# Kernel tuning notes

Measured on AMD Instinct MI355X. Metric: run time of the kernel, lower is better.

The kernel has to match this reference:

```python
import jax, jax.numpy as jnp
import numpy as np

BN_EPS = 1e-5


def _conv1x1(w, x):
    # w: [out, in], x: [B, in, N] -> [B, out, N]
    return jnp.einsum('oi,bin->bon', w, x)


def _bn_eval(x, g, b, m, v):
    # x: [B, C, N]; eval-mode BatchNorm1d with running stats
    scale = (g / jnp.sqrt(v + BN_EPS))[None, :, None]
    shift = (b - m * g / jnp.sqrt(v + BN_EPS))[None, :, None]
    return x * scale + shift


def _sa_layer(x, xyz, wqk, wv, bvv, wt, btt, g, b2, m, v):
    # offset-attention (SALayerCLS). q_conv and k_conv share weights -> q == k.
    h = x + xyz                                   # [B, C, N]
    q = _conv1x1(wqk, h)                          # [B, C//4, N]
    val = _conv1x1(wv, h) + bvv[None, :, None]    # [B, C, N]
    energy = jnp.einsum('bdn,bdm->bnm', q, q)     # [B, N, N]
    att = jax.nn.softmax(energy, axis=-1)
    # double normalization: L1-renormalize over dim=1 (rows)
    att = att / (1e-9 + att.sum(axis=1, keepdims=True))
    x_r = jnp.einsum('bcn,bnm->bcm', val, att)    # [B, C, N]
    t = _conv1x1(wt, x - x_r) + btt[None, :, None]
    t = jax.nn.relu(_bn_eval(t, g, b2, m, v))
    return x + t


def setup_inputs() -> dict:
    key = jax.random.key(0)
    ks = jax.random.split(key, 17)
    B, C, N = 8, 256, 2048
    f = jnp.float32
    return {
        'x': jax.random.normal(ks[0], (B, C, N), f),
        'xyz': jax.random.normal(ks[1], (B, N, 3), f),
        'conv1_w': jax.random.normal(ks[2], (C, C), f) * 0.05,
        'convpos_w': jax.random.normal(ks[3], (C, 3), f) * 0.05,
        'bn1_g': jax.random.uniform(ks[4], (C,), f, 0.5, 1.5),
        'bn1_b': jax.random.normal(ks[5], (C,), f) * 0.05,
        'bn1_m': jax.random.normal(ks[6], (C,), f) * 0.05,
        'bn1_v': jax.random.uniform(ks[7], (C,), f, 0.5, 1.5),
        'Wqk': jax.random.normal(ks[8], (4, C // 4, C), f) * 0.05,
        'Wv': jax.random.normal(ks[9], (4, C, C), f) * 0.05,
        'bv': jax.random.normal(ks[10], (4, C), f) * 0.05,
        'Wt': jax.random.normal(ks[11], (4, C, C), f) * 0.05,
        'bt': jax.random.normal(ks[12], (4, C), f) * 0.05,
        'bn_g': jax.random.uniform(ks[13], (4, C), f, 0.5, 1.5),
        'bn_b': jax.random.normal(ks[14], (4, C), f) * 0.05,
        'bn_m': jax.random.normal(ks[15], (4, C), f) * 0.05,
        'bn_v': jax.random.uniform(ks[16], (4, C), f, 0.5, 1.5),
    }


def reference(x, xyz, conv1_w, convpos_w, bn1_g, bn1_b, bn1_m, bn1_v,
              Wqk, Wv, bv, Wt, bt, bn_g, bn_b, bn_m, bn_v):
    # xyz: [B, N, 3] -> conv_pos -> [B, C, N]
    pos = jnp.einsum('oi,bni->bon', convpos_w, xyz)
    h = jax.nn.relu(_bn_eval(_conv1x1(conv1_w, x), bn1_g, bn1_b, bn1_m, bn1_v))
    outs = []
    for i in range(4):  # four stacked SA layers (structurally distinct params)
        h = _sa_layer(h, pos, Wqk[i], Wv[i], bv[i], Wt[i], bt[i],
                      bn_g[i], bn_b[i], bn_m[i], bn_v[i])
        outs.append(h)
    return jnp.concatenate(outs, axis=1)  # [B, 4*C, N]
```

## Files before the change

kernel.cpp:

```cpp
#include <hip/hip_runtime.h>
#include <hip/hip_bf16.h>
#include <math.h>

#define B_DIM 8
#define C_DIM 256
#define N_DIM 2048
#define CQ 64

#define TM 64
#define TN 64
#define TK 16

#define PV_BN 32
#define PV_BK 64

using short8 = __attribute__((ext_vector_type(8))) short;
using f32x4 = __attribute__((ext_vector_type(4))) float;

__device__ __forceinline__ unsigned short f2bf(float x) {
  union { float f; unsigned int u; } c; c.f = x;
  unsigned int r = c.u + 0x7fffu + ((c.u >> 16) & 1u);
  return (unsigned short)(r >> 16);
}
__device__ __forceinline__ float bf2f(unsigned short u) {
  union { unsigned int ui; float f; } c; c.ui = ((unsigned int)u) << 16;
  return c.f;
}

__global__ void split_kernel(const float* __restrict__ src, unsigned short* __restrict__ hi,
                             unsigned short* __restrict__ lo, int count) {
  int i = blockIdx.x * 256 + threadIdx.x;
  if (i < count) {
    float v = src[i];
    unsigned short h = f2bf(v);
    hi[i] = h;
    lo[i] = f2bf(v - bf2f(h));
  }
}

__global__ void pos_kernel(const float* __restrict__ w, const float* __restrict__ xyz,
                           float* __restrict__ pos) {
  int n = blockIdx.x * blockDim.x + threadIdx.x;
  int c = blockIdx.y;
  int b = blockIdx.z;
  const float* xp = xyz + ((long long)b * N_DIM + n) * 3;
  pos[((long long)b * C_DIM + c) * N_DIM + n] =
      w[c * 3 + 0] * xp[0] + w[c * 3 + 1] * xp[1] + w[c * 3 + 2] * xp[2];
// ... 44 lines not shown
      for (int jj = 0; jj < 4; jj++) bb[jj] = Bs[k][tx * 4 + jj];
#pragma unroll
      for (int ii = 0; ii < 4; ii++)
#pragma unroll
        for (int jj = 0; jj < 4; jj++)
          acc[ii][jj] = fmaf(a[ii], bb[jj], acc[ii][jj]);
    }
    __syncthreads();
  }
#pragma unroll
  for (int ii = 0; ii < 4; ii++) {
    int m = m0 + ty * 4 + ii;
    float sh = bias ? bias[m] : 0.f;
    bool dobn = (bng != nullptr);
    float bnsc = 0.f, bnsh = 0.f;
    if (dobn) {
      bnsc = bng[m] * rsqrtf(bnv[m] + 1e-5f);
      bnsh = bnb[m] - bnm[m] * bnsc;
    }
#pragma unroll
    for (int jj = 0; jj < 4; jj++) {
      int n = n0 + tx * 4 + jj;
      float v = acc[ii][jj] + sh;
      if (dobn) v = fmaxf(v * bnsc + bnsh, 0.f);
      if (Res) v += Res[(long long)b * srB + (long long)m * N + n];
      if (Ybf)
        Ybf[(long long)b * syB + (long long)m * N + n] = f2bf(v);
      else
        Y[(long long)b * syB + (long long)m * N + n] = v;
    }
  }
}

__global__ __launch_bounds__(256) void gemm_mfma(
    const unsigned short* __restrict__ Whi, const unsigned short* __restrict__ Wlo,
    const float* __restrict__ X, long long sxB,
    const float* __restrict__ Xadd, long long saB,
    const float* __restrict__ bias,
    const float* __restrict__ bng, const float* __restrict__ bnb,
    const float* __restrict__ bnm, const float* __restrict__ bnv,
    const float* __restrict__ Res, long long srB,
    float* __restrict__ Y, unsigned short* __restrict__ Ybf, long long syB) {
  const int N = N_DIM, K = C_DIM;
  int b = blockIdx.z;
  int m0 = blockIdx.y * 128;
  int n0 = blockIdx.x * 64;
  int t = threadIdx.x;
  int w = t >> 6, l = t & 63;
  int lr = l & 15, lk = l >> 4;
  int j = t & 63, dq = t >> 6;
  int ar = t >> 3, as_ = t & 7;

  __shared__ __align__(16) char Ah[128 * 128];
  __shared__ __align__(16) char Al[128 * 128];
  __shared__ __align__(16) char Bh[64 * 128];
  __shared__ __align__(16) char Bl[64 * 128];

  const float* Xb = X + (long long)b * sxB;
  const float* Adb = Xadd ? Xadd + (long long)b * saB : nullptr;

  f32x4 acc[2][4];
#pragma unroll
  for (int i = 0; i < 2; i++)
#pragma unroll
    for (int jq = 0; jq < 4; jq++) acc[i][jq] = f32x4{0.f, 0.f, 0.f, 0.f};

  for (int k0 = 0; k0 < K; k0 += 64) {
    short8 wh[4], wl[4];
#pragma unroll
    for (int it = 0; it < 4; it++) {
      int r = it * 32 + ar;
      wh[it] = *(const short8*)(Whi + (long long)(m0 + r) * K + k0 + as_ * 8);
      wl[it] = *(const short8*)(Wlo + (long long)(m0 + r) * K + k0 + as_ * 8);
    }
    float v[16];
#pragma unroll
    for (int i = 0; i < 16; i++) {
      float x = Xb[(long long)(k0 + dq * 16 + i) * N + n0 + j];
      if (Adb) x += Adb[(long long)(k0 + dq * 16 + i) * N + n0 + j];
      v[i] = x;
    }
    unsigned int ph[8], pl[8];
#pragma unroll
    for (int i = 0; i < 8; i++) {
      unsigned short h0 = f2bf(v[2 * i]), h1 = f2bf(v[2 * i + 1]);
      unsigned short l0 = f2bf(v[2 * i] - bf2f(h0)), l1 = f2bf(v[2 * i + 1] - bf2f(h1));
      ph[i] = (unsigned int)h0 | ((unsigned int)h1 << 16);
      pl[i] = (unsigned int)l0 | ((unsigned int)l1 << 16);
    }
#pragma unroll
    for (int it = 0; it < 4; it++) {
      int r = it * 32 + ar;
      *(short8*)(Ah + r * 128 + ((as_ ^ (r & 7)) << 4)) = wh[it];
      *(short8*)(Al + r * 128 + ((as_ ^ (r & 7)) << 4)) = wl[it];
    }
    {
      int o0 = dq * 2, o1 = dq * 2 + 1;
      *(uint4*)(Bh + j * 128 + ((o0 ^ (j & 7)) << 4)) = make_uint4(ph[0], ph[1], ph[2], ph[3]);
      *(uint4*)(Bh + j * 128 + ((o1 ^ (j & 7)) << 4)) = make_uint4(ph[4], ph[5], ph[6], ph[7]);
      *(uint4*)(Bl + j * 128 + ((o0 ^ (j & 7)) << 4)) = make_uint4(pl[0], pl[1], pl[2], pl[3]);
      *(uint4*)(Bl + j * 128 + ((o1 ^ (j & 7)) << 4)) = make_uint4(pl[4], pl[5], pl[6], pl[7]);
    }
    __syncthreads();
#pragma unroll
    for (int sub = 0; sub < 2; sub++) {
      short8 ah[2], al2[2], bh[4], bl[4];
#pragma unroll
      for (int mi = 0; mi < 2; mi++) {
        int ra = w * 32 + mi * 16 + lr;
        ah[mi] = *(const short8*)(Ah + ra * 128 + (((sub * 4 + lk) ^ (ra & 7)) << 4));
        al2[mi] = *(const short8*)(Al + ra * 128 + (((sub * 4 + lk) ^ (ra & 7)) << 4));
      }
#pragma unroll
      for (int ni = 0; ni < 4; ni++) {
        int rb = ni * 16 + lr;
        bh[ni] = *(const short8*)(Bh + rb * 128 + (((sub * 4 + lk) ^ (rb & 7)) << 4));
        bl[ni] = *(const short8*)(Bl + rb * 128 + (((sub * 4 + lk) ^ (rb & 7)) << 4));
      }
#pragma unroll
      for (int mi = 0; mi < 2; mi++)
#pragma unroll
        for (int ni = 0; ni < 4; ni++) {
          acc[mi][ni] = __builtin_amdgcn_mfma_f32_16x16x32_bf16(ah[mi], bh[ni], acc[mi][ni], 0, 0, 0);
          acc[mi][ni] = __builtin_amdgcn_mfma_f32_16x16x32_bf16(ah[mi], bl[ni], acc[mi][ni], 0, 0, 0);
          acc[mi][ni] = __builtin_amdgcn_mfma_f32_16x16x32_bf16(al2[mi], bh[ni], acc[mi][ni], 0, 0, 0);
        }
    }
    __syncthreads();
  }
#pragma unroll
  for (int mi = 0; mi < 2; mi++) {
#pragma unroll
    for (int jj = 0; jj < 4; jj++) {
      int m = m0 + w * 32 + mi * 16 + lk * 4 + jj;
      float sh = bias ? bias[m] : 0.f;
      bool dobn = (bng != nullptr);
      float bnsc = 0.f, bnsh = 0.f;
      if (dobn) {
        bnsc = bng[m] * rsqrtf(bnv[m] + 1e-5f);
        bnsh = bnb[m] - bnm[m] * bnsc;
      }
#pragma unroll
      for (int ni = 0; ni < 4; ni++) {
        int n = n0 + ni * 16 + lr;
        float vv = acc[mi][ni][jj] + sh;
        if (dobn) vv = fmaxf(vv * bnsc + bnsh, 0.f);
        if (Res) vv += Res[(long long)b * srB + (long long)m * N + n];
        if (Ybf)
          Ybf[(long long)b * syB + (long long)m * N + n] = f2bf(vv);
        else
          Y[(long long)b * syB + (long long)m * N + n] = vv;
      }
    }
  }
}

__global__ __launch_bounds__(256) void energy_mfma(const float* __restrict__ q,
                                                   float* __restrict__ E,
                                                   float2* __restrict__ Epart) {
  const int N = N_DIM;
  int b = blockIdx.z;
  int r0 = blockIdx.y * 64;
  int c0 = blockIdx.x * 64;
  int t = threadIdx.x;
  int w = t >> 6, l = t & 63;
  int lr = l & 15, lk = l >> 4;
  int j = t & 63, dq = t >> 6;

  __shared__ __align__(16) char Ah[64 * 128];
  __shared__ __align__(16) char Al[64 * 128];
  __shared__ __align__(16) char Bh[64 * 128];
  __shared__ __align__(16) char Bl[64 * 128];

  const float* qb = q + (long long)b * CQ * N;
  {
    float va[16], vb[16];
#pragma unroll
    for (int i = 0; i < 16; i++) {
      va[i] = qb[(long long)(dq * 16 + i) * N + r0 + j];
      vb[i] = qb[(long long)(dq * 16 + i) * N + c0 + j];
    }
    unsigned int pah[8], pal[8], pbh[8], pbl[8];
#pragma unroll
    for (int i = 0; i < 8; i++) {
      unsigned short h0 = f2bf(va[2 * i]), h1 = f2bf(va[2 * i + 1]);
      unsigned short l0 = f2bf(va[2 * i] - bf2f(h0)), l1 = f2bf(va[2 * i + 1] - bf2f(h1));
      pah[i] = (unsigned int)h0 | ((unsigned int)h1 << 16);
      pal[i] = (unsigned int)l0 | ((unsigned int)l1 << 16);
      unsigned short g0 = f2bf(vb[2 * i]), g1 = f2bf(vb[2 * i + 1]);
      unsigned short m0_ = f2bf(vb[2 * i] - bf2f(g0)), m1 = f2bf(vb[2 * i + 1] - bf2f(g1));
      pbh[i] = (unsigned int)g0 | ((unsigned int)g1 << 16);
      pbl[i] = (unsigned int)m0_ | ((unsigned int)m1 << 16);
    }
    int o0 = dq * 2, o1 = dq * 2 + 1;
    *(uint4*)(Ah + j * 128 + ((o0 ^ (j & 7)) << 4)) = make_uint4(pah[0], pah[1], pah[2], pah[3]);
    *(uint4*)(Ah + j * 128 + ((o1 ^ (j & 7)) << 4)) = make_uint4(pah[4], pah[5], pah[6], pah[7]);
    *(uint4*)(Al + j * 128 + ((o0 ^ (j & 7)) << 4)) = make_uint4(pal[0], pal[1], pal[2], pal[3]);
    *(uint4*)(Al + j * 128 + ((o1 ^ (j & 7)) << 4)) = make_uint4(pal[4], pal[5], pal[6], pal[7]);
    *(uint4*)(Bh + j * 128 + ((o0 ^ (j & 7)) << 4)) = make_uint4(pbh[0], pbh[1], pbh[2], pbh[3]);
    *(uint4*)(Bh + j * 128 + ((o1 ^ (j & 7)) << 4)) = make_uint4(pbh[4], pbh[5], pbh[6], pbh[7]);
    *(uint4*)(Bl + j * 128 + ((o0 ^ (j & 7)) << 4)) = make_uint4(pbl[0], pbl[1], pbl[2], pbl[3]);
    *(uint4*)(Bl + j * 128 + ((o1 ^ (j & 7)) << 4)) = make_uint4(pbl[4], pbl[5], pbl[6], pbl[7]);
  }
  __syncthreads();

  f32x4 acc[4];
#pragma unroll
  for (int i = 0; i < 4; i++) acc[i] = f32x4{0.f, 0.f, 0.f, 0.f};
#pragma unroll
  for (int sub = 0; sub < 2; sub++) {
    int ra = w * 16 + lr;
    short8 ah = *(const short8*)(Ah + ra * 128 + (((sub * 4 + lk) ^ (ra & 7)) << 4));
    short8 al = *(const short8*)(Al + ra * 128 + (((sub * 4 + lk) ^ (ra & 7)) << 4));
    short8 bh[4], bl[4];
#pragma unroll
    for (int ni = 0; ni < 4; ni++) {
      int rb = ni * 16 + lr;
      bh[ni] = *(const short8*)(Bh + rb * 128 + (((sub * 4 + lk) ^ (rb & 7)) << 4));
      bl[ni] = *(const short8*)(Bl + rb * 128 + (((sub * 4 + lk) ^ (rb & 7)) << 4));
    }
#pragma unroll
    for (int ni = 0; ni < 4; ni++) {
      acc[ni] = __builtin_amdgcn_mfma_f32_16x16x32_bf16(ah, bh[ni], acc[ni], 0, 0, 0);
      acc[ni] = __builtin_amdgcn_mfma_f32_16x16x32_bf16(ah, bl[ni], acc[ni], 0, 0, 0);
      acc[ni] = __builtin_amdgcn_mfma_f32_16x16x32_bf16(al, bh[ni], acc[ni], 0, 0, 0);
    }
  }
  long long base = (long long)b * N * N;
#pragma unroll
  for (int ni = 0; ni < 4; ni++)
#pragma unroll
    for (int jj = 0; jj < 4; jj++)
      E[base + (long long)(r0 + w * 16 + lk * 4 + jj) * N + c0 + ni * 16 + lr] = acc[ni][jj];

  const long long BNr = (long long)B_DIM * N_DIM;
#pragma unroll
  for (int jj = 0; jj < 4; jj++) {
    float m = fmaxf(fmaxf(acc[0][jj], acc[1][jj]), fmaxf(acc[2][jj], acc[3][jj]));
#pragma unroll
    for (int msk = 1; msk < 16; msk <<= 1) m = fmaxf(m, __shfl_xor(m, msk, 64));
    float s = 0.f;
#pragma unroll
    for (int ni = 0; ni < 4; ni++) s += __expf(acc[ni][jj] - m);
#pragma unroll
    for (int msk = 1; msk < 16; msk <<= 1) s += __shfl_xor(s, msk, 64);
    if (lr == 0) {
      long long row = (long long)b * N + r0 + w * 16 + lk * 4 + jj;
      Epart[(long long)(c0 >> 6) * BNr + row] = make_float2(m, s);
    }
  }
}

__global__ void rowstats2(const float2* __restrict__ Epart, float* __restrict__ rmax,
                          float* __restrict__ rinv) {
  const long long BNr = (long long)B_DIM * N_DIM;
  int rloc = threadIdx.x & 63, qd = threadIdx.x >> 6;
  long long row = (long long)blockIdx.x * 64 + rloc;
  float2 v[8];
  float m = -3.4e38f;
#pragma unroll
  for (int i = 0; i < 8; i++) {
    v[i] = Epart[(long long)(qd * 8 + i) * BNr + row];
    m = fmaxf(m, v[i].x);
  }
  float s = 0.f;
#pragma unroll
  for (int i = 0; i < 8; i++) s += v[i].y * __expf(v[i].x - m);
  __shared__ float sm[4][64], ss[4][64];
  sm[qd][rloc] = m;
  ss[qd][rloc] = s;
  __syncthreads();
  if (qd == 0) {
    float M = fmaxf(fmaxf(sm[0][rloc], sm[1][rloc]), fmaxf(sm[2][rloc], sm[3][rloc]));
    float S = ss[0][rloc] * __expf(sm[0][rloc] - M) + ss[1][rloc] * __expf(sm[1][rloc] - M) +
              ss[2][rloc] * __expf(sm[2][rloc] - M) + ss[3][rloc] * __expf(sm[3][rloc] - M);
    rmax[row] = M;
    rinv[row] = 1.0f / S;
  }
}

__global__ __launch_bounds__(256) void pv_mfma(
    const unsigned short* __restrict__ valbf,
    const float* __restrict__ E,
    const float* __restrict__ rmax, const float* __restrict__ rinv,
    const float* __restrict__ Hprev, long long shB, float* __restrict__ D) {
  const int N = N_DIM;
  int b = blockIdx.z;
  int n0 = blockIdx.x * PV_BN;
  int t = threadIdx.x;
  int w = t >> 6, l = t & 63;
  int lr = l & 15, lk = l >> 4;
  int brow = t >> 3, bkq = t & 7;
  int ar = t >> 3, as_ = t & 7;

  __shared__ __align__(16) char As[C_DIM * PV_BK * 2];
  __shared__ __align__(16) char Bs[PV_BN * PV_BK * 2];
  __shared__ float csred[8][PV_BN];
  __shared__ float csfin[PV_BN];

  const unsigned short* vb = valbf + (long long)b * C_DIM * N;
  const float* Ebr = E + ((long long)b * N + n0 + brow) * N;
  const float* rm = rmax + (long long)b * N;
  const float* ri = rinv + (long long)b * N;

  f32x4 acc[4][2];
#pragma unroll
  for (int i = 0; i < 4; i++)
#pragma unroll
    for (int jq = 0; jq < 2; jq++) acc[i][jq] = f32x4{0.f, 0.f, 0.f, 0.f};
  float cs = 0.f;

  float4 ev[2], rv[2], iv[2];
#pragma unroll
  for (int it = 0; it < 2; it++) {
    int kl = bkq * 4 + it * 32;
    ev[it] = *(const float4*)(Ebr + kl);
    rv[it] = *(const float4*)(rm + kl);
    iv[it] = *(const float4*)(ri + kl);
  }

  for (int k0 = 0; k0 < N; k0 += PV_BK) {
    short8 areg[8];
#pragma unroll
    for (int it = 0; it < 8; it++) {
      int r = it * 32 + ar;
      areg[it] = *(const short8*)(vb + (long long)r * N + k0 + as_ * 8);
    }
#pragma unroll
    for (int it = 0; it < 2; it++) {
      int kl = bkq * 4 + it * 32;
      float a0 = __expf(ev[it].x - rv[it].x) * iv[it].x;
      float a1 = __expf(ev[it].y - rv[it].y) * iv[it].y;
      float a2 = __expf(ev[it].z - rv[it].z) * iv[it].z;
      float a3 = __expf(ev[it].w - rv[it].w) * iv[it].w;
      unsigned short u0 = f2bf(a0), u1 = f2bf(a1), u2 = f2bf(a2), u3 = f2bf(a3);
      cs += bf2f(u0) + bf2f(u1) + bf2f(u2) + bf2f(u3);
      uint2 pk;
      pk.x = (unsigned int)u0 | ((unsigned int)u1 << 16);
      pk.y = (unsigned int)u2 | ((unsigned int)u3 << 16);
      *(uint2*)(Bs + brow * 128 + ((((kl >> 3) ^ (brow & 7)) << 4) | ((kl & 7) * 2))) = pk;
    }
#pragma unroll
    for (int it = 0; it < 8; it++) {
      int r = it * 32 + ar;
      *(short8*)(As + r * 128 + ((as_ ^ (r & 7)) << 4)) = areg[it];
    }
    __syncthreads();
    if (k0 + PV_BK < N) {
      int kb = k0 + PV_BK;
#pragma unroll
      for (int it = 0; it < 2; it++) {
        int kl = bkq * 4 + it * 32;
        ev[it] = *(const float4*)(Ebr + kb + kl);
        rv[it] = *(const float4*)(rm + kb + kl);
        iv[it] = *(const float4*)(ri + kb + kl);
      }
    }
#pragma unroll
    for (int sub = 0; sub < 2; sub++) {
      short8 af[4], bq[2];
#pragma unroll
      for (int ni = 0; ni < 2; ni++) {
        int r = ni * 16 + lr;
        bq[ni] = *(const short8*)(Bs + r * 128 + (((sub * 4 + lk) ^ (r & 7)) << 4));
      }
#pragma unroll
      for (int mi = 0; mi < 4; mi++) {
        int r = w * 64 + mi * 16 + lr;
        af[mi] = *(const short8*)(As + r * 128 + (((sub * 4 + lk) ^ (r & 7)) << 4));
      }
#pragma unroll
      for (int mi = 0; mi < 4; mi++)
#pragma unroll
        for (int ni = 0; ni < 2; ni++)
          acc[mi][ni] =
              __builtin_amdgcn_mfma_f32_16x16x32_bf16(af[mi], bq[ni], acc[mi][ni], 0, 0, 0);
    }
    __syncthreads();
  }

  csred[bkq][brow] = cs;
  __syncthreads();
  if (t < PV_BN) {
    float s = 0.f;
#pragma unroll
    for (int i = 0; i < 8; i++) s += csred[i][t];
    csfin[t] = s;
  }
  __syncthreads();

  const float* Hb = Hprev + (long long)b * shB;
  float* Db = D + (long long)b * C_DIM * N;
#pragma unroll
  for (int mi = 0; mi < 4; mi++) {
#pragma unroll
    for (int ni = 0; ni < 2; ni++) {
#pragma unroll
      for (int jj = 0; jj < 4; jj++) {
        int cr = w * 64 + mi * 16 + lk * 4 + jj;
        int ml = ni * 16 + lr;
        float denom = 1e-9f + csfin[ml];
        float xr = acc[mi][ni][jj] / denom;
        Db[(long long)cr * N + n0 + ml] = Hb[(long long)cr * N + n0 + ml] - xr;
      }
    }
  }
}

extern "C" void kernel_launch(void* const* d_in, const int* in_sizes, int n_in,
                              void* d_out, int out_size, void* d_ws, size_t ws_size,
                              hipStream_t stream) {
  const float* x = (const float*)d_in[0];
  const float* xyz = (const float*)d_in[1];
  const float* conv1_w = (const float*)d_in[2];
  const float* convpos_w = (const float*)d_in[3];
  const float* bn1_g = (const float*)d_in[4];
  const float* bn1_b = (const float*)d_in[5];
  const float* bn1_m = (const float*)d_in[6];
  const float* bn1_v = (const float*)d_in[7];
  const float* Wqk = (const float*)d_in[8];
  const float* Wv = (const float*)d_in[9];
  const float* bv = (const float*)d_in[10];
  const float* Wt = (const float*)d_in[11];
  const float* bt = (const float*)d_in[12];
  const float* bng = (const float*)d_in[13];
  const float* bnb = (const float*)d_in[14];
  const float* bnm = (const float*)d_in[15];
  const float* bnv = (const float*)d_in[16];
  float* out = (float*)d_out;

  const long long BCN = (long long)B_DIM * C_DIM * N_DIM;
  const long long CN = (long long)C_DIM * N_DIM;
  const long long BN = (long long)B_DIM * N_DIM;
  const int WSZ = C_DIM * C_DIM;
  float* ws = (float*)d_ws;
  float* pos = ws;
  float* h0 = pos + BCN;
  float* qbuf = h0 + BCN;
  float* dbuf = qbuf + (long long)B_DIM * CQ * N_DIM;
  float* rmax = dbuf + BCN;
  float* rinv = rmax + BN;
  unsigned short* valbf = (unsigned short*)(rinv + BN);
  unsigned short* whi = valbf + BCN;
  unsigned short* wlo = whi + 9 * WSZ;
  float2* Epart = (float2*)(wlo + 9 * WSZ);
  float* E = (float*)(Epart + 32 * BN);

  unsigned short* c1hi = whi;
  unsigned short* c1lo = wlo;
  unsigned short* wvhi = whi + WSZ;
  unsigned short* wvlo = wlo + WSZ;
  unsigned short* wthi = whi + 5 * WSZ;
  unsigned short* wtlo = wlo + 5 * WSZ;

  dim3 blk(256);

  split_kernel<<<dim3(WSZ / 256), blk, 0, stream>>>(conv1_w, c1hi, c1lo, WSZ);
  split_kernel<<<dim3(4 * WSZ / 256), blk, 0, stream>>>(Wv, wvhi, wvlo, 4 * WSZ);
  split_kernel<<<dim3(4 * WSZ / 256), blk, 0, stream>>>(Wt, wthi, wtlo, 4 * WSZ);

  pos_kernel<<<dim3(N_DIM / 256, C_DIM, B_DIM), blk, 0, stream>>>(convpos_w, xyz, pos);

  gemm_mfma<<<dim3(N_DIM / 64, 2, B_DIM), blk, 0, stream>>>(
      c1hi, c1lo, x, CN, nullptr, 0, nullptr,
      bn1_g, bn1_b, bn1_m, bn1_v, nullptr, 0, h0, nullptr, CN);

  for (int i = 0; i < 4; i++) {
    const float* hp = (i == 0) ? h0 : out + (long long)(i - 1) * CN;
    long long shp = (i == 0) ? CN : 4 * CN;

    gemm_wx<<<dim3(N_DIM / TN, CQ / TM, B_DIM), blk, 0, stream>>>(
        Wqk + (long long)i * CQ * C_DIM, hp, shp, pos, CN, nullptr,
        nullptr, nullptr, nullptr, nullptr, nullptr, 0,
        qbuf, nullptr, (long long)CQ * N_DIM, CQ, C_DIM);

    gemm_mfma<<<dim3(N_DIM / 64, 2, B_DIM), blk, 0, stream>>>(
        wvhi + (long long)i * WSZ, wvlo + (long long)i * WSZ, hp, shp, pos, CN,
        bv + i * C_DIM, nullptr, nullptr, nullptr, nullptr, nullptr, 0,
        nullptr, valbf, CN);

    energy_mfma<<<dim3(N_DIM / 64, N_DIM / 64, B_DIM), blk, 0, stream>>>(qbuf, E, Epart);

    rowstats2<<<dim3(B_DIM * N_DIM / 64), blk, 0, stream>>>(Epart, rmax, rinv);

    pv_mfma<<<dim3(N_DIM / PV_BN, 1, B_DIM), blk, 0, stream>>>(
        valbf, E, rmax, rinv, hp, shp, dbuf);

    gemm_mfma<<<dim3(N_DIM / 64, 2, B_DIM), blk, 0, stream>>>(
        wthi + (long long)i * WSZ, wtlo + (long long)i * WSZ, dbuf, CN, nullptr, 0,
        bt + i * C_DIM, bng + i * C_DIM, bnb + i * C_DIM, bnm + i * C_DIM, bnv + i * C_DIM,
        hp, shp, out + (long long)i * CN, nullptr, 4 * CN);
  }
}
```

Measured before the change: 826.8 us.

## Recompute energy in PV kernel instead of materializing the full N×N matrix

The energy kernel no longer writes the B×N×N fp32 energy matrix. A new stats kernel loops over 16 column tiles per block and keeps an online max and sum, producing two partials per row. The PV kernel recomputes each energy tile from q with split-bf16 MFMAs, then applies exp and normalization in place. This removes a large global write and read of E, at the cost of computing the energy GEMM twice and giving the PV kernel more per-iteration work and more syncs.

```diff
diff --git a/kernel.cpp b/kernel.cpp
--- a/kernel.cpp
+++ b/kernel.cpp
@@ -11,8 +11,7 @@
 #define TN 64
 #define TK 16
 
-#define PV_BN 32
-#define PV_BK 64
+#define NT 32
 
 using short8 = __attribute__((ext_vector_type(8))) short;
 using f32x4 = __attribute__((ext_vector_type(4))) float;
@@ -246,98 +245,104 @@
   }
 }
 
-__global__ __launch_bounds__(256) void energy_mfma(const float* __restrict__ q,
-                                                   float* __restrict__ E,
-                                                   float2* __restrict__ Epart) {
+__global__ __launch_bounds__(256) void qstats(const float* __restrict__ q,
+                                              float2* __restrict__ Epart) {
   const int N = N_DIM;
   int b = blockIdx.z;
-  int r0 = blockIdx.y * 64;
-  int c0 = blockIdx.x * 64;
+  int r0 = blockIdx.x * 64;
+  int cz = blockIdx.y;
   int t = threadIdx.x;
   int w = t >> 6, l = t & 63;
   int lr = l & 15, lk = l >> 4;
   int j = t & 63, dq = t >> 6;
 
-  __shared__ __align__(16) char Ah[64 * 128];
-  __shared__ __align__(16) char Al[64 * 128];
-  __shared__ __align__(16) char Bh[64 * 128];
-  __shared__ __align__(16) char Bl[64 * 128];
+  __shared__ __align__(16) char Arh[64 * 128], Arl[64 * 128];
+  __shared__ __align__(16) char Bch[64 * 128], Bcl[64 * 128];
 
   const float* qb = q + (long long)b * CQ * N;
   {
-    float va[16], vb[16];
-#pragma unroll
-    for (int i = 0; i < 16; i++) {
-      va[i] = qb[(long long)(dq * 16 + i) * N + r0 + j];
-      vb[i] = qb[(long long)(dq * 16 + i) * N + c0 + j];
-    }
-    unsigned int pah[8], pal[8], pbh[8], pbl[8];
+    float va[16];
+#pragma unroll
+    for (int i = 0; i < 16; i++) va[i] = qb[(long long)(dq * 16 + i) * N + r0 + j];
+    unsigned int ph[8], pl[8];
 #pragma unroll
     for (int i = 0; i < 8; i++) {
       unsigned short h0 = f2bf(va[2 * i]), h1 = f2bf(va[2 * i + 1]);
       unsigned short l0 = f2bf(va[2 * i] - bf2f(h0)), l1 = f2bf(va[2 * i + 1] - bf2f(h1));
-      pah[i] = (unsigned int)h0 | ((unsigned int)h1 << 16);
-      pal[i] = (unsigned int)l0 | ((unsigned int)l1 << 16);
-      unsigned short g0 = f2bf(vb[2 * i]), g1 = f2bf(vb[2 * i + 1]);
-      unsigned short m0_ = f2bf(vb[2 * i] - bf2f(g0)), m1 = f2bf(vb[2 * i + 1] - bf2f(g1));
-      pbh[i] = (unsigned int)g0 | ((unsigned int)g1 << 16);
-      pbl[i] = (unsigned int)m0_ | ((unsigned int)m1 << 16);
+      ph[i] = (unsigned int)h0 | ((unsigned int)h1 << 16);
+      pl[i] = (unsigned int)l0 | ((unsigned int)l1 << 16);
     }
     int o0 = dq * 2, o1 = dq * 2 + 1;
-    *(uint4*)(Ah + j * 128 + ((o0 ^ (j & 7)) << 4)) = make_uint4(pah[0], pah[1], pah[2], pah[3]);
-    *(uint4*)(Ah + j * 128 + ((o1 ^ (j & 7)) << 4)) = make_uint4(pah[4], pah[5], pah[6], pah[7]);
-    *(uint4*)(Al + j * 128 + ((o0 ^ (j & 7)) << 4)) = make_uint4(pal[0], pal[1], pal[2], pal[3]);
-    *(uint4*)(Al + j * 128 + ((o1 ^ (j & 7)) << 4)) = make_uint4(pal[4], pal[5], pal[6], pal[7]);
-    *(uint4*)(Bh + j * 128 + ((o0 ^ (j & 7)) << 4)) = make_uint4(pbh[0], pbh[1], pbh[2], pbh[3]);
-    *(uint4*)(Bh + j * 128 + ((o1 ^ (j & 7)) << 4)) = make_uint4(pbh[4], pbh[5], pbh[6], pbh[7]);
-    *(uint4*)(Bl + j * 128 + ((o0 ^ (j & 7)) << 4)) = make_uint4(pbl[0], pbl[1], pbl[2], pbl[3]);
-    *(uint4*)(Bl + j * 128 + ((o1 ^ (j & 7)) << 4)) = make_uint4(pbl[4], pbl[5], pbl[6], pbl[7]);
-  }
-  __syncthreads();
-
-  f32x4 acc[4];
-#pragma unroll
-  for (int i = 0; i < 4; i++) acc[i] = f32x4{0.f, 0.f, 0.f, 0.f};
-#pragma unroll
-  for (int sub = 0; sub < 2; sub++) {
-    int ra = w * 16 + lr;
-    short8 ah = *(const short8*)(Ah + ra * 128 + (((sub * 4 + lk) ^ (ra & 7)) << 4));
-    short8 al = *(const short8*)(Al + ra * 128 + (((sub * 4 + lk) ^ (ra & 7)) << 4));
-    short8 bh[4], bl[4];
-#pragma unroll
-    for (int ni = 0; ni < 4; ni++) {
-      int rb = ni * 16 + lr;
-      bh[ni] = *(const short8*)(Bh + rb * 128 + (((sub * 4 + lk) ^ (rb & 7)) << 4));
-      bl[ni] = *(const short8*)(Bl + rb * 128 + (((sub * 4 + lk) ^ (rb & 7)) << 4));
-    }
-#pragma unroll
-    for (int ni = 0; ni < 4; ni++) {
-      acc[ni] = __builtin_amdgcn_mfma_f32_16x16x32_bf16(ah, bh[ni], acc[ni], 0, 0, 0);
-      acc[ni] = __builtin_amdgcn_mfma_f32_16x16x32_bf16(ah, bl[ni], acc[ni], 0, 0, 0);
-      acc[ni] = __builtin_amdgcn_mfma_f32_16x16x32_bf16(al, bh[ni], acc[ni], 0, 0, 0);
-    }
-  }
-  long long base = (long long)b * N * N;
-#pragma unroll
-  for (int ni = 0; ni < 4; ni++)
-#pragma unroll
-    for (int jj = 0; jj < 4; jj++)
-      E[base + (long long)(r0 + w * 16 + lk * 4 + jj) * N + c0 + ni * 16 + lr] = acc[ni][jj];
-
-  const long long BNr = (long long)B_DIM * N_DIM;
-#pragma unroll
-  for (int jj = 0; jj < 4; jj++) {
-    float m = fmaxf(fmaxf(acc[0][jj], acc[1][jj]), fmaxf(acc[2][jj], acc[3][jj]));
-#pragma unroll
-    for (int msk = 1; msk < 16; msk <<= 1) m = fmaxf(m, __shfl_xor(m, msk, 64));
-    float s = 0.f;
-#pragma unroll
-    for (int ni = 0; ni < 4; ni++) s += __expf(acc[ni][jj] - m);
-#pragma unroll
-    for (int msk = 1; msk < 16; msk <<= 1) s += __shfl_xor(s, msk, 64);
-    if (lr == 0) {
+    *(uint4*)(Arh + j * 128 + ((o0 ^ (j & 7)) << 4)) = make_uint4(ph[0], ph[1], ph[2], ph[3]);
+    *(uint4*)(Arh + j * 128 + ((o1 ^ (j & 7)) << 4)) = make_uint4(ph[4], ph[5], ph[6], ph[7]);
+    *(uint4*)(Arl + j * 128 + ((o0 ^ (j & 7)) << 4)) = make_uint4(pl[0], pl[1], pl[2], pl[3]);
+    *(uint4*)(Arl + j * 128 + ((o1 ^ (j & 7)) << 4)) = make_uint4(pl[4], pl[5], pl[6], pl[7]);
+  }
+
+  float m[4], s[4];
+#pragma unroll
+  for (int jj = 0; jj < 4; jj++) { m[jj] = -3.0e38f; s[jj] = 0.f; }
+
+  for (int ct = 0; ct < 16; ct++) {
+    int c0 = (cz * 16 + ct) * 64;
+    float vb_[16];
+#pragma unroll
+    for (int i = 0; i < 16; i++) vb_[i] = qb[(long long)(dq * 16 + i) * N + c0 + j];
+    unsigned int ph[8], pl[8];
+#pragma unroll
+    for (int i = 0; i < 8; i++) {
+      unsigned short h0 = f2bf(vb_[2 * i]), h1 = f2bf(vb_[2 * i + 1]);
+      unsigned short l0 = f2bf(vb_[2 * i] - bf2f(h0)), l1 = f2bf(vb_[2 * i + 1] - bf2f(h1));
+      ph[i] = (unsigned int)h0 | ((unsigned int)h1 << 16);
+      pl[i] = (unsigned int)l0 | ((unsigned int)l1 << 16);
+    }
+    __syncthreads();
+    {
+      int o0 = dq * 2, o1 = dq * 2 + 1;
+      *(uint4*)(Bch + j * 128 + ((o0 ^ (j & 7)) << 4)) = make_uint4(ph[0], ph[1], ph[2], ph[3]);
+      *(uint4*)(Bch + j * 128 + ((o1 ^ (j & 7)) << 4)) = make_uint4(ph[4], ph[5], ph[6], ph[7]);
+      *(uint4*)(Bcl + j * 128 + ((o0 ^ (j & 7)) << 4)) = make_uint4(pl[0], pl[1], pl[2], pl[3]);
+      *(uint4*)(Bcl + j * 128 + ((o1 ^ (j & 7)) << 4)) = make_uint4(pl[4], pl[5], pl[6], pl[7]);
+    }
+    __syncthreads();
+    f32x4 e[4];
+#pragma unroll
+    for (int ni = 0; ni < 4; ni++) e[ni] = f32x4{0.f, 0.f, 0.f, 0.f};
+#pragma unroll
+    for (int sub = 0; sub < 2; sub++) {
+      int ra = w * 16 + lr;
+      short8 ah = *(const short8*)(Arh + ra * 128 + (((sub * 4 + lk) ^ (ra & 7)) << 4));
+      short8 al = *(const short8*)(Arl + ra * 128 + (((sub * 4 + lk) ^ (ra & 7)) << 4));
+#pragma unroll
+      for (int ni = 0; ni < 4; ni++) {
+        int rb = ni * 16 + lr;
+        short8 bh = *(const short8*)(Bch + rb * 128 + (((sub * 4 + lk) ^ (rb & 7)) << 4));
+        short8 bl = *(const short8*)(Bcl + rb * 128 + (((sub * 4 + lk) ^ (rb & 7)) << 4));
+        e[ni] = __builtin_amdgcn_mfma_f32_16x16x32_bf16(ah, bh, e[ni], 0, 0, 0);
+        e[ni] = __builtin_amdgcn_mfma_f32_16x16x32_bf16(ah, bl, e[ni], 0, 0, 0);
+        e[ni] = __builtin_amdgcn_mfma_f32_16x16x32_bf16(al, bh, e[ni], 0, 0, 0);
+      }
+    }
+#pragma unroll
+    for (int jj = 0; jj < 4; jj++) {
+      float vmax = fmaxf(fmaxf(e[0][jj], e[1][jj]), fmaxf(e[2][jj], e[3][jj]));
+#pragma unroll
+      for (int msk = 1; msk < 16; msk <<= 1) vmax = fmaxf(vmax, __shfl_xor(vmax, msk, 64));
+      float ssum = 0.f;
+#pragma unroll
+      for (int ni = 0; ni < 4; ni++) ssum += __expf(e[ni][jj] - vmax);
+#pragma unroll
+      for (int msk = 1; msk < 16; msk <<= 1) ssum += __shfl_xor(ssum, msk, 64);
+      float Mn = fmaxf(m[jj], vmax);
+      s[jj] = s[jj] * __expf(m[jj] - Mn) + ssum * __expf(vmax - Mn);
+      m[jj] = Mn;
+    }
+  }
+  if (lr == 0) {
+#pragma unroll
+    for (int jj = 0; jj < 4; jj++) {
       long long row = (long long)b * N + r0 + w * 16 + lk * 4 + jj;
-      Epart[(long long)(c0 >> 6) * BNr + row] = make_float2(m, s);
+      Epart[(long long)cz * ((long long)B_DIM * N) + row] = make_float2(m[jj], s[jj]);
     }
   }
 }
@@ -345,111 +350,132 @@
 __global__ void rowstats2(const float2* __restrict__ Epart, float* __restrict__ rmax,
                           float* __restrict__ rinv) {
   const long long BNr = (long long)B_DIM * N_DIM;
-  int rloc = threadIdx.x & 63, qd = threadIdx.x >> 6;
-  long long row = (long long)blockIdx.x * 64 + rloc;
-  float2 v[8];
-  float m = -3.4e38f;
-#pragma unroll
-  for (int i = 0; i < 8; i++) {
-    v[i] = Epart[(long long)(qd * 8 + i) * BNr + row];
-    m = fmaxf(m, v[i].x);
-  }
-  float s = 0.f;
-#pragma unroll
-  for (int i = 0; i < 8; i++) s += v[i].y * __expf(v[i].x - m);
-  __shared__ float sm[4][64], ss[4][64];
-  sm[qd][rloc] = m;
-  ss[qd][rloc] = s;
-  __syncthreads();
-  if (qd == 0) {
-    float M = fmaxf(fmaxf(sm[0][rloc], sm[1][rloc]), fmaxf(sm[2][rloc], sm[3][rloc]));
-    float S = ss[0][rloc] * __expf(sm[0][rloc] - M) + ss[1][rloc] * __expf(sm[1][rloc] - M) +
-              ss[2][rloc] * __expf(sm[2][rloc] - M) + ss[3][rloc] * __expf(sm[3][rloc] - M);
-    rmax[row] = M;
-    rinv[row] = 1.0f / S;
-  }
-}
-
-__global__ __launch_bounds__(256) void pv_mfma(
-    const unsigned short* __restrict__ valbf,
-    const float* __restrict__ E,
+  long long row = (long long)blockIdx.x * 256 + threadIdx.x;
+  float2 a = Epart[row], c = Epart[BNr + row];
+  float M = fmaxf(a.x, c.x);
+  float S = a.y * __expf(a.x - M) + c.y * __expf(c.x - M);
+  rmax[row] = M;
+  rinv[row] = 1.0f / S;
+}
+
+__global__ __launch_bounds__(256) void pv_fused(
+    const float* __restrict__ q, const unsigned short* __restrict__ valbf,
     const float* __restrict__ rmax, const float* __restrict__ rinv,
     const float* __restrict__ Hprev, long long shB, float* __restrict__ D) {
   const int N = N_DIM;
   int b = blockIdx.z;
-  int n0 = blockIdx.x * PV_BN;
+  int n0 = blockIdx.x * NT;
   int t = threadIdx.x;
   int w = t >> 6, l = t & 63;
   int lr = l & 15, lk = l >> 4;
-  int brow = t >> 3, bkq = t & 7;
+  int jq = t & 63, dq = t >> 6;
+  int j2 = t & 31, dg = t >> 5;
   int ar = t >> 3, as_ = t & 7;
 
-  __shared__ __align__(16) char As[C_DIM * PV_BK * 2];
-  __shared__ __align__(16) char Bs[PV_BN * PV_BK * 2];
-  __shared__ float csred[8][PV_BN];
-  __shared__ float csfin[PV_BN];
-
+  __shared__ __align__(16) char Qnh[NT * 128], Qnl[NT * 128];
+  __shared__ __align__(16) char Qkh[64 * 128], Qkl[64 * 128];
+  __shared__ __align__(16) char As[C_DIM * 128];
+  __shared__ __align__(16) char Bs[NT * 128];
+  __shared__ float csred[4][NT];
+  __shared__ float csfin[NT];
+
+  const float* qb = q + (long long)b * CQ * N;
   const unsigned short* vb = valbf + (long long)b * C_DIM * N;
-  const float* Ebr = E + ((long long)b * N + n0 + brow) * N;
   const float* rm = rmax + (long long)b * N;
   const float* ri = rinv + (long long)b * N;
 
+  {
+    float va[8];
+#pragma unroll
+    for (int i = 0; i < 8; i++) va[i] = qb[(long long)(dg * 8 + i) * N + n0 + j2];
+    short8 h8, l8;
+#pragma unroll
+    for (int i = 0; i < 8; i++) {
+      unsigned short h = f2bf(va[i]);
+      h8[i] = (short)h;
+      l8[i] = (short)f2bf(va[i] - bf2f(h));
+    }
+    *(short8*)(Qnh + j2 * 128 + ((dg ^ (j2 & 7)) << 4)) = h8;
+    *(short8*)(Qnl + j2 * 128 + ((dg ^ (j2 & 7)) << 4)) = l8;
+  }
+
   f32x4 acc[4][2];
 #pragma unroll
   for (int i = 0; i < 4; i++)
 #pragma unroll
-    for (int jq = 0; jq < 2; jq++) acc[i][jq] = f32x4{0.f, 0.f, 0.f, 0.f};
-  float cs = 0.f;
-
-  float4 ev[2], rv[2], iv[2];
-#pragma unroll
-  for (int it = 0; it < 2; it++) {
-    int kl = bkq * 4 + it * 32;
-    ev[it] = *(const float4*)(Ebr + kl);
-    rv[it] = *(const float4*)(rm + kl);
-    iv[it] = *(const float4*)(ri + kl);
-  }
-
-  for (int k0 = 0; k0 < N; k0 += PV_BK) {
+    for (int jj = 0; jj < 2; jj++) acc[i][jj] = f32x4{0.f, 0.f, 0.f, 0.f};
+  float cs[2] = {0.f, 0.f};
+  __syncthreads();
+
+  for (int k0 = 0; k0 < N; k0 += 64) {
+    float vq[16];
+#pragma unroll
+    for (int i = 0; i < 16; i++) vq[i] = qb[(long long)(dq * 16 + i) * N + k0 + jq];
     short8 areg[8];
+#pragma unroll
+    for (int it = 0; it < 8; it++)
+      areg[it] = *(const short8*)(vb + (long long)(it * 32 + ar) * N + k0 + as_ * 8);
+    float4 rm4 = *(const float4*)(rm + k0 + w * 16 + lk * 4);
+    float4 ri4 = *(const float4*)(ri + k0 + w * 16 + lk * 4);
+    unsigned int ph[8], pl[8];
+#pragma unroll
+    for (int i = 0; i < 8; i++) {
+      unsigned short h0 = f2bf(vq[2 * i]), h1 = f2bf(vq[2 * i + 1]);
+      unsigned short l0 = f2bf(vq[2 * i] - bf2f(h0)), l1 = f2bf(vq[2 * i + 1] - bf2f(h1));
+      ph[i] = (unsigned int)h0 | ((unsigned int)h1 << 16);
+      pl[i] = (unsigned int)l0 | ((unsigned int)l1 << 16);
+    }
+    __syncthreads();
+    {
+      int o0 = dq * 2, o1 = dq * 2 + 1;
+      *(uint4*)(Qkh + jq * 128 + ((o0 ^ (jq & 7)) << 4)) = make_uint4(ph[0], ph[1], ph[2], ph[3]);
+      *(uint4*)(Qkh + jq * 128 + ((o1 ^ (jq & 7)) << 4)) = make_uint4(ph[4], ph[5], ph[6], ph[7]);
+      *(uint4*)(Qkl + jq * 128 + ((o0 ^ (jq & 7)) << 4)) = make_uint4(pl[0], pl[1], pl[2], pl[3]);
+      *(uint4*)(Qkl + jq * 128 + ((o1 ^ (jq & 7)) << 4)) = make_uint4(pl[4], pl[5], pl[6], pl[7]);
+    }
 #pragma unroll
     for (int it = 0; it < 8; it++) {
       int r = it * 32 + ar;
-      areg[it] = *(const short8*)(vb + (long long)r * N + k0 + as_ * 8);
-    }
-#pragma unroll
-    for (int it = 0; it < 2; it++) {
-      int kl = bkq * 4 + it * 32;
-      float a0 = __expf(ev[it].x - rv[it].x) * iv[it].x;
-      float a1 = __expf(ev[it].y - rv[it].y) * iv[it].y;
-      float a2 = __expf(ev[it].z - rv[it].z) * iv[it].z;
-      float a3 = __expf(ev[it].w - rv[it].w) * iv[it].w;
+      *(short8*)(As + r * 128 + ((as_ ^ (r & 7)) << 4)) = areg[it];
+    }
+    __syncthreads();
+    f32x4 e[2];
+    e[0] = f32x4{0.f, 0.f, 0.f, 0.f};
+    e[1] = f32x4{0.f, 0.f, 0.f, 0.f};
+#pragma unroll
+    for (int sub = 0; sub < 2; sub++) {
+      int ra = w * 16 + lr;
+      short8 ah = *(const short8*)(Qkh + ra * 128 + (((sub * 4 + lk) ^ (ra & 7)) << 4));
+      short8 al = *(const short8*)(Qkl + ra * 128 + (((sub * 4 + lk) ^ (ra & 7)) << 4));
+#pragma unroll
+      for (int ni = 0; ni < 2; ni++) {
+        int rb = ni * 16 + lr;
+        short8 bh = *(const short8*)(Qnh + rb * 128 + (((sub * 4 + lk) ^ (rb & 7)) << 4));
+        short8 bl = *(const short8*)(Qnl + rb * 128 + (((sub * 4 + lk) ^ (rb & 7)) << 4));
+        e[ni] = __builtin_amdgcn_mfma_f32_16x16x32_bf16(ah, bh, e[ni], 0, 0, 0);
+        e[ni] = __builtin_amdgcn_mfma_f32_16x16x32_bf16(ah, bl, e[ni], 0, 0, 0);
+        e[ni] = __builtin_amdgcn_mfma_f32_16x16x32_bf16(al, bh, e[ni], 0, 0, 0);
+      }
+    }
+    int kl = w * 16 + lk * 4;
+#pragma unroll
+    for (int ni = 0; ni < 2; ni++) {
+      float a0 = __expf(e[ni][0] - rm4.x) * ri4.x;
+      float a1 = __expf(e[ni][1] - rm4.y) * ri4.y;
+      float a2 = __expf(e[ni][2] - rm4.z) * ri4.z;
+      float a3 = __expf(e[ni][3] - rm4.w) * ri4.w;
       unsigned short u0 = f2bf(a0), u1 = f2bf(a1), u2 = f2bf(a2), u3 = f2bf(a3);
-      cs += bf2f(u0) + bf2f(u1) + bf2f(u2) + bf2f(u3);
+      cs[ni] += bf2f(u0) + bf2f(u1) + bf2f(u2) + bf2f(u3);
       uint2 pk;
       pk.x = (unsigned int)u0 | ((unsigned int)u1 << 16);
       pk.y = (unsigned int)u2 | ((unsigned int)u3 << 16);
-      *(uint2*)(Bs + brow * 128 + ((((kl >> 3) ^ (brow & 7)) << 4) | ((kl & 7) * 2))) = pk;
-    }
-#pragma unroll
-    for (int it = 0; it < 8; it++) {
-      int r = it * 32 + ar;
-      *(short8*)(As + r * 128 + ((as_ ^ (r & 7)) << 4)) = areg[it];
-    }
-    __syncthreads();
-    if (k0 + PV_BK < N) {
-      int kb = k0 + PV_BK;
-#pragma unroll
-      for (int it = 0; it < 2; it++) {
-        int kl = bkq * 4 + it * 32;
-        ev[it] = *(const float4*)(Ebr + kb + kl);
-        rv[it] = *(const float4*)(rm + kb + kl);
-        iv[it] = *(const float4*)(ri + kb + kl);
-      }
-    }
+      int n = ni * 16 + lr;
+      *(uint2*)(Bs + n * 128 + ((((kl >> 3) ^ (n & 7)) << 4) | ((kl & 7) * 2))) = pk;
+    }
+    __syncthreads();
 #pragma unroll
     for (int sub = 0; sub < 2; sub++) {
-      short8 af[4], bq[2];
+      short8 bq[2];
 #pragma unroll
       for (int ni = 0; ni < 2; ni++) {
         int r = ni * 16 + lr;
@@ -458,26 +484,24 @@
 #pragma unroll
       for (int mi = 0; mi < 4; mi++) {
         int r = w * 64 + mi * 16 + lr;
-        af[mi] = *(const short8*)(As + r * 128 + (((sub * 4 + lk) ^ (r & 7)) << 4));
-      }
-#pragma unroll
-      for (int mi = 0; mi < 4; mi++)
+        short8 af = *(const short8*)(As + r * 128 + (((sub * 4 + lk) ^ (r & 7)) << 4));
 #pragma unroll
         for (int ni = 0; ni < 2; ni++)
-          acc[mi][ni] =
-              __builtin_amdgcn_mfma_f32_16x16x32_bf16(af[mi], bq[ni], acc[mi][ni], 0, 0, 0);
-    }
-    __syncthreads();
-  }
-
-  csred[bkq][brow] = cs;
+          acc[mi][ni] = __builtin_amdgcn_mfma_f32_16x16x32_bf16(af, bq[ni], acc[mi][ni], 0, 0, 0);
+      }
+    }
+  }
+
+  cs[0] += __shfl_xor(cs[0], 16, 64);
+  cs[0] += __shfl_xor(cs[0], 32, 64);
+  cs[1] += __shfl_xor(cs[1], 16, 64);
+  cs[1] += __shfl_xor(cs[1], 32, 64);
+  if (lk == 0) {
+    csred[w][lr] = cs[0];
+    csred[w][16 + lr] = cs[1];
+  }
   __syncthreads();
-  if (t < PV_BN) {
-    float s = 0.f;
-#pragma unroll
-    for (int i = 0; i < 8; i++) s += csred[i][t];
-    csfin[t] = s;
-  }
+  if (t < NT) csfin[t] = csred[0][t] + csred[1][t] + csred[2][t] + csred[3][t];
   __syncthreads();
 
   const float* Hb = Hprev + (long long)b * shB;
@@ -535,7 +559,6 @@
   unsigned short* whi = valbf + BCN;
   unsigned short* wlo = whi + 9 * WSZ;
   float2* Epart = (float2*)(wlo + 9 * WSZ);
-  float* E = (float*)(Epart + 32 * BN);
 
   unsigned short* c1hi = whi;
   unsigned short* c1lo = wlo;
@@ -570,12 +593,11 @@
         bv + i * C_DIM, nullptr, nullptr, nullptr, nullptr, nullptr, 0,
         nullptr, valbf, CN);
 
-    energy_mfma<<<dim3(N_DIM / 64, N_DIM / 64, B_DIM), blk, 0, stream>>>(qbuf, E, Epart);
-
-    rowstats2<<<dim3(B_DIM * N_DIM / 64), blk, 0, stream>>>(Epart, rmax, rinv);
-
-    pv_mfma<<<dim3(N_DIM / PV_BN, 1, B_DIM), blk, 0, stream>>>(
-        valbf, E, rmax, rinv, hp, shp, dbuf);
+    qstats<<<dim3(N_DIM / 64, 2, B_DIM), blk, 0, stream>>>(qbuf, Epart);
+    rowstats2<<<dim3(B_DIM * N_DIM / 256), blk, 0, stream>>>(Epart, rmax, rinv);
+
+    pv_fused<<<dim3(N_DIM / NT, 1, B_DIM), blk, 0, stream>>>(
+        qbuf, valbf, rmax, rinv, hp, shp, dbuf);
 
     gemm_mfma<<<dim3(N_DIM / 64, 2, B_DIM), blk, 0, stream>>>(
         wthi + (long long)i * WSZ, wtlo + (long long)i * WSZ, dbuf, CN, nullptr, 0,
```

After: 928.4 us. +12.3%, slower.

## Restructure PV kernel to 512 threads and drop X-lo term in value GEMM

Applied to the files above, without the earlier changes.

The PV kernel now uses 512-thread blocks with 8 waves, each owning 32 channel rows. E-tile loads are spread over 16 threads per row, and the column sum is reduced with wave shuffles into a reciprocal instead of a shared-memory pass. The value GEMM, whose output is stored as bf16, gets a template flag that skips the X-low split term, cutting one third of its MFMAs and a shared buffer. This trades a little precision in the value projection and adds a sync at the top of the PV loop.

```diff
diff --git a/kernel.cpp b/kernel.cpp
--- a/kernel.cpp
+++ b/kernel.cpp
@@ -11,8 +11,7 @@
 #define TN 64
 #define TK 16
 
-#define PV_BN 32
-#define PV_BK 64
+#define NT 32
 
 using short8 = __attribute__((ext_vector_type(8))) short;
 using f32x4 = __attribute__((ext_vector_type(4))) float;
@@ -123,6 +122,7 @@
   }
 }
 
+template <bool XLO>
 __global__ __launch_bounds__(256) void gemm_mfma(
     const unsigned short* __restrict__ Whi, const unsigned short* __restrict__ Wlo,
     const float* __restrict__ X, long long sxB,
@@ -145,7 +145,7 @@
   __shared__ __align__(16) char Ah[128 * 128];
   __shared__ __align__(16) char Al[128 * 128];
   __shared__ __align__(16) char Bh[64 * 128];
-  __shared__ __align__(16) char Bl[64 * 128];
+  __shared__ __align__(16) char Bl[XLO ? 64 * 128 : 16];
 
   const float* Xb = X + (long long)b * sxB;
   const float* Adb = Xadd ? Xadd + (long long)b * saB : nullptr;
@@ -175,9 +175,11 @@
 #pragma unroll
     for (int i = 0; i < 8; i++) {
       unsigned short h0 = f2bf(v[2 * i]), h1 = f2bf(v[2 * i + 1]);
-      unsigned short l0 = f2bf(v[2 * i] - bf2f(h0)), l1 = f2bf(v[2 * i + 1] - bf2f(h1));
       ph[i] = (unsigned int)h0 | ((unsigned int)h1 << 16);
-      pl[i] = (unsigned int)l0 | ((unsigned int)l1 << 16);
+      if (XLO) {
+        unsigned short l0 = f2bf(v[2 * i] - bf2f(h0)), l1 = f2bf(v[2 * i + 1] - bf2f(h1));
+        pl[i] = (unsigned int)l0 | ((unsigned int)l1 << 16);
+      }
     }
 #pragma unroll
     for (int it = 0; it < 4; it++) {
@@ -189,8 +191,10 @@
       int o0 = dq * 2, o1 = dq * 2 + 1;
       *(uint4*)(Bh + j * 128 + ((o0 ^ (j & 7)) << 4)) = make_uint4(ph[0], ph[1], ph[2], ph[3]);
       *(uint4*)(Bh + j * 128 + ((o1 ^ (j & 7)) << 4)) = make_uint4(ph[4], ph[5], ph[6], ph[7]);
-      *(uint4*)(Bl + j * 128 + ((o0 ^ (j & 7)) << 4)) = make_uint4(pl[0], pl[1], pl[2], pl[3]);
-      *(uint4*)(Bl + j * 128 + ((o1 ^ (j & 7)) << 4)) = make_uint4(pl[4], pl[5], pl[6], pl[7]);
+      if (XLO) {
+        *(uint4*)(Bl + j * 128 + ((o0 ^ (j & 7)) << 4)) = make_uint4(pl[0], pl[1], pl[2], pl[3]);
+        *(uint4*)(Bl + j * 128 + ((o1 ^ (j & 7)) << 4)) = make_uint4(pl[4], pl[5], pl[6], pl[7]);
+      }
     }
     __syncthreads();
 #pragma unroll
@@ -206,14 +210,15 @@
       for (int ni = 0; ni < 4; ni++) {
         int rb = ni * 16 + lr;
         bh[ni] = *(const short8*)(Bh + rb * 128 + (((sub * 4 + lk) ^ (rb & 7)) << 4));
-        bl[ni] = *(const short8*)(Bl + rb * 128 + (((sub * 4 + lk) ^ (rb & 7)) << 4));
+        if (XLO) bl[ni] = *(const short8*)(Bl + rb * 128 + (((sub * 4 + lk) ^ (rb & 7)) << 4));
       }
 #pragma unroll
       for (int mi = 0; mi < 2; mi++)
 #pragma unroll
         for (int ni = 0; ni < 4; ni++) {
           acc[mi][ni] = __builtin_amdgcn_mfma_f32_16x16x32_bf16(ah[mi], bh[ni], acc[mi][ni], 0, 0, 0);
-          acc[mi][ni] = __builtin_amdgcn_mfma_f32_16x16x32_bf16(ah[mi], bl[ni], acc[mi][ni], 0, 0, 0);
+          if (XLO)
+            acc[mi][ni] = __builtin_amdgcn_mfma_f32_16x16x32_bf16(ah[mi], bl[ni], acc[mi][ni], 0, 0, 0);
           acc[mi][ni] = __builtin_amdgcn_mfma_f32_16x16x32_bf16(al2[mi], bh[ni], acc[mi][ni], 0, 0, 0);
         }
     }
@@ -370,60 +375,54 @@
   }
 }
 
-__global__ __launch_bounds__(256) void pv_mfma(
+__global__ __launch_bounds__(512, 4) void pv_mfma(
     const unsigned short* __restrict__ valbf,
     const float* __restrict__ E,
     const float* __restrict__ rmax, const float* __restrict__ rinv,
     const float* __restrict__ Hprev, long long shB, float* __restrict__ D) {
   const int N = N_DIM;
   int b = blockIdx.z;
-  int n0 = blockIdx.x * PV_BN;
+  int n0 = blockIdx.x * NT;
   int t = threadIdx.x;
   int w = t >> 6, l = t & 63;
   int lr = l & 15, lk = l >> 4;
-  int brow = t >> 3, bkq = t & 7;
-  int ar = t >> 3, as_ = t & 7;
-
-  __shared__ __align__(16) char As[C_DIM * PV_BK * 2];
-  __shared__ __align__(16) char Bs[PV_BN * PV_BK * 2];
-  __shared__ float csred[8][PV_BN];
-  __shared__ float csfin[PV_BN];
+  int brow = t >> 4, kq = t & 15;
+
+  __shared__ __align__(16) char As[C_DIM * 128];
+  __shared__ __align__(16) char Bs[NT * 128];
+  __shared__ float csfin[NT];
 
   const unsigned short* vb = valbf + (long long)b * C_DIM * N;
   const float* Ebr = E + ((long long)b * N + n0 + brow) * N;
   const float* rm = rmax + (long long)b * N;
   const float* ri = rinv + (long long)b * N;
 
-  f32x4 acc[4][2];
-#pragma unroll
-  for (int i = 0; i < 4; i++)
+  f32x4 acc[2][2];
+#pragma unroll
+  for (int i = 0; i < 2; i++)
 #pragma unroll
     for (int jq = 0; jq < 2; jq++) acc[i][jq] = f32x4{0.f, 0.f, 0.f, 0.f};
   float cs = 0.f;
 
-  float4 ev[2], rv[2], iv[2];
-#pragma unroll
-  for (int it = 0; it < 2; it++) {
-    int kl = bkq * 4 + it * 32;
-    ev[it] = *(const float4*)(Ebr + kl);
-    rv[it] = *(const float4*)(rm + kl);
-    iv[it] = *(const float4*)(ri + kl);
-  }
-
-  for (int k0 = 0; k0 < N; k0 += PV_BK) {
-    short8 areg[8];
-#pragma unroll
-    for (int it = 0; it < 8; it++) {
-      int r = it * 32 + ar;
-      areg[it] = *(const short8*)(vb + (long long)r * N + k0 + as_ * 8);
-    }
-#pragma unroll
-    for (int it = 0; it < 2; it++) {
-      int kl = bkq * 4 + it * 32;
-      float a0 = __expf(ev[it].x - rv[it].x) * iv[it].x;
-      float a1 = __expf(ev[it].y - rv[it].y) * iv[it].y;
-      float a2 = __expf(ev[it].z - rv[it].z) * iv[it].z;
-      float a3 = __expf(ev[it].w - rv[it].w) * iv[it].w;
+  const int kl = kq * 4;
+  float4 ev = *(const float4*)(Ebr + kl);
+  float4 rv = *(const float4*)(rm + kl);
+  float4 iv = *(const float4*)(ri + kl);
+  short8 areg[4];
+#pragma unroll
+  for (int it = 0; it < 4; it++) {
+    int idx = it * 512 + t;
+    int r = idx >> 3, s = idx & 7;
+    areg[it] = *(const short8*)(vb + (long long)r * N + s * 8);
+  }
+
+  for (int k0 = 0; k0 < N; k0 += 64) {
+    __syncthreads();
+    {
+      float a0 = __expf(ev.x - rv.x) * iv.x;
+      float a1 = __expf(ev.y - rv.y) * iv.y;
+      float a2 = __expf(ev.z - rv.z) * iv.z;
+      float a3 = __expf(ev.w - rv.w) * iv.w;
       unsigned short u0 = f2bf(a0), u1 = f2bf(a1), u2 = f2bf(a2), u3 = f2bf(a3);
       cs += bf2f(u0) + bf2f(u1) + bf2f(u2) + bf2f(u3);
       uint2 pk;
@@ -432,66 +431,61 @@
       *(uint2*)(Bs + brow * 128 + ((((kl >> 3) ^ (brow & 7)) << 4) | ((kl & 7) * 2))) = pk;
     }
 #pragma unroll
-    for (int it = 0; it < 8; it++) {
-      int r = it * 32 + ar;
-      *(short8*)(As + r * 128 + ((as_ ^ (r & 7)) << 4)) = areg[it];
+    for (int it = 0; it < 4; it++) {
+      int idx = it * 512 + t;
+      int r = idx >> 3, s = idx & 7;
+      *(short8*)(As + r * 128 + ((s ^ (r & 7)) << 4)) = areg[it];
     }
     __syncthreads();
-    if (k0 + PV_BK < N) {
-      int kb = k0 + PV_BK;
-#pragma unroll
-      for (int it = 0; it < 2; it++) {
-        int kl = bkq * 4 + it * 32;
-        ev[it] = *(const float4*)(Ebr + kb + kl);
-        rv[it] = *(const float4*)(rm + kb + kl);
-        iv[it] = *(const float4*)(ri + kb + kl);
+    if (k0 + 64 < N) {
+      int kb = k0 + 64;
+      ev = *(const float4*)(Ebr + kb + kl);
+      rv = *(const float4*)(rm + kb + kl);
+      iv = *(const float4*)(ri + kb + kl);
+#pragma unroll
+      for (int it = 0; it < 4; it++) {
+        int idx = it * 512 + t;
+        int r = idx >> 3, s = idx & 7;
+        areg[it] = *(const short8*)(vb + (long long)r * N + kb + s * 8);
       }
     }
 #pragma unroll
     for (int sub = 0; sub < 2; sub++) {
-      short8 af[4], bq[2];
+      short8 bq[2];
 #pragma unroll
       for (int ni = 0; ni < 2; ni++) {
-        int r = ni * 16 + lr;
-        bq[ni] = *(const short8*)(Bs + r * 128 + (((sub * 4 + lk) ^ (r & 7)) << 4));
-      }
-#pragma unroll
-      for (int mi = 0; mi < 4; mi++) {
-        int r = w * 64 + mi * 16 + lr;
-        af[mi] = *(const short8*)(As + r * 128 + (((sub * 4 + lk) ^ (r & 7)) << 4));
-      }
-#pragma unroll
-      for (int mi = 0; mi < 4; mi++)
+        int rn = ni * 16 + lr;
+        bq[ni] = *(const short8*)(Bs + rn * 128 + (((sub * 4 + lk) ^ (rn & 7)) << 4));
+      }
+#pragma unroll
+      for (int mi = 0; mi < 2; mi++) {
+        int ra = w * 32 + mi * 16 + lr;
+        short8 af = *(const short8*)(As + ra * 128 + (((sub * 4 + lk) ^ (ra & 7)) << 4));
 #pragma unroll
         for (int ni = 0; ni < 2; ni++)
-          acc[mi][ni] =
-              __builtin_amdgcn_mfma_f32_16x16x32_bf16(af[mi], bq[ni], acc[mi][ni], 0, 0, 0);
-    }
-    __syncthreads();
-  }
-
-  csred[bkq][brow] = cs;
-  __syncthreads();
-  if (t < PV_BN) {
-    float s = 0.f;
-#pragma unroll
-    for (int i = 0; i < 8; i++) s += csred[i][t];
-    csfin[t] = s;
-  }
+          acc[mi][ni] = __builtin_amdgcn_mfma_f32_16x16x32_bf16(af, bq[ni], acc[mi][ni], 0, 0, 0);
+      }
+    }
+  }
+
+  cs += __shfl_xor(cs, 1, 64);
+  cs += __shfl_xor(cs, 2, 64);
+  cs += __shfl_xor(cs, 4, 64);
+  cs += __shfl_xor(cs, 8, 64);
+  if (kq == 0) csfin[brow] = 1.0f / (1e-9f + cs);
   __syncthreads();
 
   const float* Hb = Hprev + (long long)b * shB;
   float* Db = D + (long long)b * C_DIM * N;
 #pragma unroll
-  for (int mi = 0; mi < 4; mi++) {
+  for (int mi = 0; mi < 2; mi++) {
 #pragma unroll
     for (int ni = 0; ni < 2; ni++) {
 #pragma unroll
       for (int jj = 0; jj < 4; jj++) {
-        int cr = w * 64 + mi * 16 + lk * 4 + jj;
+        int cr = w * 32 + mi * 16 + lk * 4 + jj;
         int ml = ni * 16 + lr;
-        float denom = 1e-9f + csfin[ml];
-        float xr = acc[mi][ni][jj] / denom;
+        float xr = acc[mi][ni][jj] * csfin[ml];
         Db[(long long)cr * N + n0 + ml] = Hb[(long long)cr * N + n0 + ml] - xr;
       }
     }
@@ -552,7 +546,7 @@
 
   pos_kernel<<<dim3(N_DIM / 256, C_DIM, B_DIM), blk, 0, stream>>>(convpos_w, xyz, pos);
 
-  gemm_mfma<<<dim3(N_DIM / 64, 2, B_DIM), blk, 0, stream>>>(
+  gemm_mfma<true><<<dim3(N_DIM / 64, 2, B_DIM), blk, 0, stream>>>(
       c1hi, c1lo, x, CN, nullptr, 0, nullptr,
       bn1_g, bn1_b, bn1_m, bn1_v, nullptr, 0, h0, nullptr, CN);
 
@@ -565,7 +559,7 @@
         nullptr, nullptr, nullptr, nullptr, nullptr, 0,
         qbuf, nullptr, (long long)CQ * N_DIM, CQ, C_DIM);
 
-    gemm_mfma<<<dim3(N_DIM / 64, 2, B_DIM), blk, 0, stream>>>(
+    gemm_mfma<false><<<dim3(N_DIM / 64, 2, B_DIM), blk, 0, stream>>>(
         wvhi + (long long)i * WSZ, wvlo + (long long)i * WSZ, hp, shp, pos, CN,
         bv + i * C_DIM, nullptr, nullptr, nullptr, nullptr, nullptr, 0,
         nullptr, valbf, CN);
@@ -574,10 +568,10 @@
 
     rowstats2<<<dim3(B_DIM * N_DIM / 64), blk, 0, stream>>>(Epart, rmax, rinv);
 
-    pv_mfma<<<dim3(N_DIM / PV_BN, 1, B_DIM), blk, 0, stream>>>(
+    pv_mfma<<<dim3(N_DIM / NT, 1, B_DIM), dim3(512), 0, stream>>>(
         valbf, E, rmax, rinv, hp, shp, dbuf);
 
-    gemm_mfma<<<dim3(N_DIM / 64, 2, B_DIM), blk, 0, stream>>>(
+    gemm_mfma<true><<<dim3(N_DIM / 64, 2, B_DIM), blk, 0, stream>>>(
         wthi + (long long)i * WSZ, wtlo + (long long)i * WSZ, dbuf, CN, nullptr, 0,
         bt + i * C_DIM, bng + i * C_DIM, bnb + i * C_DIM, bnm + i * C_DIM, bnv + i * C_DIM,
         hp, shp, out + (long long)i * CN, nullptr, 4 * CN);
```

Result: no change. 813.6 us (-1.6%).
